# Kernel tuning notes

Hardware: AMD Instinct MI355X
Metric: run time of the kernel (lower is better)

## Reference

```python
import jax, jax.numpy as jnp
import numpy as np

B, S, D = 2, 2048, 2048
H = 16
Q_LORA, KV_LORA = 1536, 512
ROPE_DIM, NOPE_DIM, V_DIM = 64, 64, 128
Q_HEAD_DIM = NOPE_DIM + ROPE_DIM  # 128
ROPE_THETA, ROPE_RATIO = 10000.0, 1.0


def setup_inputs() -> dict:
    key = jax.random.key(0)
    ks = jax.random.split(key, 6)
    std = 0.02
    return {
        "hidden_states": jax.random.normal(ks[0], (B, S, D), jnp.float32),
        "Wqa": jax.random.normal(ks[1], (D, Q_LORA), jnp.float32) * std,
        "Wqb": jax.random.normal(ks[2], (Q_LORA, H * Q_HEAD_DIM), jnp.float32) * std,
        "Wkva": jax.random.normal(ks[3], (D, KV_LORA + ROPE_DIM), jnp.float32) * std,
        "Wkvb": jax.random.normal(ks[4], (KV_LORA, H * (NOPE_DIM + V_DIM)), jnp.float32) * std,
        "Wo": jax.random.normal(ks[5], (H * V_DIM, D), jnp.float32) * std,
    }


def _rope_tables(seq_len):
    half = ROPE_DIM // 2
    inv_freq = ROPE_RATIO / (ROPE_THETA ** (jnp.arange(half, dtype=jnp.float32) * 2.0 / ROPE_DIM))
    freqs = jnp.arange(seq_len, dtype=jnp.float32)[:, None] * inv_freq[None, :]  # [S, half]
    return jnp.cos(freqs), jnp.sin(freqs)


def _apply_rope(x, cos, sin):
    # interleaved even/odd rotation, matches torch stack+flatten
    x_even = x[..., 0::2]
    x_odd = x[..., 1::2]
    r_even = x_even * cos - x_odd * sin
    r_odd = x_odd * cos + x_even * sin
    return jnp.stack([r_even, r_odd], axis=-1).reshape(x.shape)


def reference(hidden_states, Wqa, Wqb, Wkva, Wkvb, Wo):
    b, s, _ = hidden_states.shape
    scale = Q_HEAD_DIM ** -0.5

    # query compression path
    q_latent = hidden_states @ Wqa                             # [B,S,Q_LORA]
    q = (q_latent @ Wqb).reshape(b, s, H, Q_HEAD_DIM)
    q = jnp.transpose(q, (0, 2, 1, 3))                          # [B,H,S,q_head_dim]
    q_nope, q_pe = q[..., :NOPE_DIM], q[..., NOPE_DIM:]

    # kv compression
    kv_comp = hidden_states @ Wkva                              # [B,S,KV_LORA+ROPE]
    c_kv, k_pe = kv_comp[..., :KV_LORA], kv_comp[..., KV_LORA:]

    cos, sin = _rope_tables(s)                                  # [S, ROPE_DIM//2]
    q_pe = _apply_rope(q_pe, cos, sin)                          # [B,H,S,ROPE]
    k_pe = _apply_rope(k_pe, cos, sin)                          # [B,S,ROPE]

    # kv decompression
    kv = (c_kv @ Wkvb).reshape(b, s, H, NOPE_DIM + V_DIM)
    kv = jnp.transpose(kv, (0, 2, 1, 3))                        # [B,H,S,nope+v]
    k_nope, v = kv[..., :NOPE_DIM], kv[..., NOPE_DIM:]

    k_pe_b = jnp.broadcast_to(k_pe[:, None], (b, H, s, ROPE_DIM))
    q_full = jnp.concatenate([q_nope, q_pe], axis=-1)           # [B,H,S,128]
    k_full = jnp.concatenate([k_nope, k_pe_b], axis=-1)         # [B,H,S,128]

    scores = jnp.einsum('bhqd,bhkd->bhqk', q_full, k_full) * scale
    causal = jnp.tril(jnp.ones((s, s), dtype=bool))
    scores = jnp.where(causal[None, None], scores, jnp.finfo(scores.dtype).min)
    probs = jax.nn.softmax(scores, axis=-1)
    attn = jnp.einsum('bhqk,bhkd->bhqd', probs, v)              # [B,H,S,V_DIM]

    out = jnp.transpose(attn, (0, 2, 1, 3)).reshape(b, s, H * V_DIM)
    return out @ Wo                                             # [B,S,D]
```

## Files before the change

kernel.cpp:

```cpp
#include <hip/hip_runtime.h>
#include <hip/hip_bf16.h>
#include <cstdint>
#include <cstddef>

typedef __bf16 bf16_t;
typedef __attribute__((ext_vector_type(4))) __bf16 bf16x4;
typedef __attribute__((ext_vector_type(8))) __bf16 bf16x8;
typedef __attribute__((ext_vector_type(4))) float f32x4;

#define S_ 2048
#define H_ 16
#define NTOK 4096

__device__ __forceinline__ f32x4 mfma16x16(bf16x8 a, bf16x8 b, f32x4 c) {
  return __builtin_amdgcn_mfma_f32_16x16x32_bf16(a, b, c, 0, 0, 0);
}
__device__ __forceinline__ bf16x8 load8(const bf16_t* p) {
  return *reinterpret_cast<const bf16x8*>(p);
}
__device__ __forceinline__ void load_lds16(const void* g, void* l) {
  __builtin_amdgcn_global_load_lds(
      (const __attribute__((address_space(1))) uint32_t*)g,
      (__attribute__((address_space(3))) uint32_t*)l, 16, 0, 0);
}


__global__ void cast_bf16_k(const float* __restrict__ in, bf16_t* __restrict__ out, int n) {
  int idx = blockIdx.x * 256 + threadIdx.x;
  int i4 = idx * 4;
  if (i4 >= n) return;
  float4 v = *reinterpret_cast<const float4*>(in + i4);
  out[i4 + 0] = (bf16_t)v.x;
  out[i4 + 1] = (bf16_t)v.y;
  out[i4 + 2] = (bf16_t)v.z;
  out[i4 + 3] = (bf16_t)v.w;
}

__global__ void rope_tables_k(float* __restrict__ cosT, float* __restrict__ sinT) {
  int idx = blockIdx.x * 256 + threadIdx.x;
  if (idx >= S_ * 32) return;
  int s = idx >> 5, i = idx & 31;
  float inv = powf(10000.0f, -(2.0f * (float)i) / 64.0f);
  float fr = (float)s * inv;
  cosT[idx] = cosf(fr);
  sinT[idx] = sinf(fr);
}

struct TDesc {
  const float* src;
  bf16_t* dst;
  int K, Nsrc, bxc, off, perm;
};
struct TDesc5 {
  TDesc d[5];
};

__global__ void transpose_cast_multi_k(TDesc5 ds) {
  __shared__ float tile[32][33];
  const int bid = blockIdx.x;
  int i = 0;
#pragma unroll
  for (int j = 1; j < 5; ++j)
    if (bid >= ds.d[j].off) i = j;
  const float* __restrict__ in = ds.d[i].src;
  bf16_t* __restrict__ out = ds.d[i].dst;
  const int K = ds.d[i].K, Nsrc = ds.d[i].Nsrc;
  const int local = bid - ds.d[i].off;
  const int n0 = (local % ds.d[i].bxc) * 32;
  const int k0 = (local / ds.d[i].bxc) * 32;
  int srcn0 = n0;
  if (ds.d[i].perm) {
    srcn0 = (n0 < 1024) ? ((n0 >> 6) * 192 + (n0 & 63))
                        : (((n0 - 1024) >> 7) * 192 + 64 + ((n0 - 1024) & 127));
  }
  int tx = threadIdx.x & 31, ty = threadIdx.x >> 5;
#pragma unroll
  for (int r = 0; r < 4; ++r) {
    int k = k0 + ty + r * 8, n = srcn0 + tx;
    tile[ty + r * 8][tx] = (n < Nsrc) ? in[(size_t)k * Nsrc + n] : 0.0f;
  }
  __syncthreads();
#pragma unroll
  for (int r = 0; r < 4; ++r) {
    int n = n0 + ty + r * 8, k = k0 + tx;
    out[(size_t)n * K + k] = (bf16_t)tile[tx][ty + r * 8];
  }
}


__device__ __forceinline__ void gemm_loop(const bf16_t* __restrict__ A, int lda,
                                          const bf16_t* __restrict__ Bt, int K, int m0, int n0,
                                          int tid, bf16_t* Al, bf16_t* Bl, f32x4 (&acc)[4][4]) {
  const int wid = tid >> 6, lane = tid & 63;
  const int wm = (wid >> 1) * 64, wn = (wid & 1) * 64;
  const int srow = wid * 32 + (lane >> 2);
  const int scol = (lane & 3) * 8;
  const bf16_t* ag0 = A + (size_t)(m0 + srow) * lda + scol;
  const bf16_t* ag1 = A + (size_t)(m0 + srow + 16) * lda + scol;
  const bf16_t* bg0 = Bt + (size_t)(n0 + srow) * K + scol;
  const bf16_t* bg1 = Bt + (size_t)(n0 + srow + 16) * K + scol;
  bf16_t* al0 = &Al[wid * 1024];
  bf16_t* al1 = &Al[wid * 1024 + 512];
  bf16_t* bl0 = &Bl[wid * 1024];
  bf16_t* bl1 = &Bl[wid * 1024 + 512];
  const int lr = lane & 15, lk = (lane >> 4) * 8;

  for (int k0 = 0; k0 < K; k0 += 32) {
    load_lds16(ag0 + k0, al0);
    load_lds16(ag1 + k0, al1);
    load_lds16(bg0 + k0, bl0);
    load_lds16(bg1 + k0, bl1);
    __syncthreads();
    bf16x8 af[4], bfr[4];
#pragma unroll
    for (int i = 0; i < 4; ++i) {
      af[i] = load8(&Al[(wm + i * 16 + lr) * 32 + lk]);
      bfr[i] = load8(&Bl[(wn + i * 16 + lr) * 32 + lk]);
    }
#pragma unroll
    for (int i = 0; i < 4; ++i)
#pragma unroll
      for (int j = 0; j < 4; ++j) acc[i][j] = mfma16x16(af[i], bfr[j], acc[i][j]);
    __syncthreads();
  }
}


__global__ __launch_bounds__(256) void gemm_lat_k(const bf16_t* __restrict__ A,
                                                  const bf16_t* __restrict__ Bt,
                                                  bf16_t* __restrict__ C,
                                                  const float* __restrict__ cosT,
                                                  const float* __restrict__ sinT) {
  __shared__ alignas(16) bf16_t Al[128 * 32];
  __shared__ alignas(16) bf16_t Bl[128 * 32];
  const int tid = threadIdx.x;
  const int m0 = blockIdx.y * 128, n0 = blockIdx.x * 128;
  f32x4 acc[4][4] = {};
  gemm_loop(A, 2048, Bt, 2048, m0, n0, tid, Al, Bl, acc);

  const int wid = tid >> 6, lane = tid & 63;
  const int wm = (wid >> 1) * 64, wn = (wid & 1) * 64;
  const int lr = lane & 15, lg = lane >> 4;
  const bool rope = (n0 == 2048) && (wn == 0);
  const int ir_base = lr >> 1;
  const bool odd = lane & 1;
#pragma unroll
  for (int i = 0; i < 4; ++i)
#pragma unroll
    for (int j = 0; j < 4; ++j) {
      float v4[4];
#pragma unroll
      for (int r = 0; r < 4; ++r) v4[r] = acc[i][j][r];
      if (rope) {
        const int ir = j * 8 + ir_base;
#pragma unroll
        for (int r = 0; r < 4; ++r) {
          const int srow_ = (m0 + wm + i * 16 + lg * 4 + r) & (S_ - 1);
          float c = cosT[srow_ * 32 + ir], sn = sinT[srow_ * 32 + ir];
          float partner = __shfl_xor(v4[r], 1);
          v4[r] = odd ? (v4[r] * c + partner * sn) : (v4[r] * c - partner * sn);
        }
      }
#pragma unroll
      for (int r = 0; r < 4; ++r) {
        int row = m0 + wm + i * 16 + lg * 4 + r;
        int col = n0 + wn + j * 16 + lr;
        C[(size_t)row * 2176 + col] = (bf16_t)v4[r];
      }
    }
}


__global__ __launch_bounds__(256) void gemm_qkv_k(const bf16_t* __restrict__ lat,
                                                  const bf16_t* __restrict__ Wqbt,
                                                  const bf16_t* __restrict__ Wkvbt,
                                                  bf16_t* __restrict__ qb,
                                                  bf16_t* __restrict__ knb,
                                                  bf16_t* __restrict__ vT,
                                                  const float* __restrict__ cosT,
                                                  const float* __restrict__ sinT, float qscale) {
  __shared__ alignas(16) bf16_t Al[128 * 32];
  __shared__ alignas(16) bf16_t Bl[128 * 32];
  const int tid = threadIdx.x;
  const int bid = blockIdx.x;
  const int wid = tid >> 6, lane = tid & 63;
  const int wm = (wid >> 1) * 64, wn = (wid & 1) * 64;
  const int lr = lane & 15, lg = lane >> 4;
  f32x4 acc[4][4] = {};

  if (bid < 512) {
    const int m0 = (bid >> 4) * 128, n0 = (bid & 15) * 128;
    gemm_loop(lat, 2176, Wqbt, 1536, m0, n0, tid, Al, Bl, acc);
    const bool rope = (wn == 64);
    const int ir_base = lr >> 1;
    const bool odd = lane & 1;
#pragma unroll
    for (int i = 0; i < 4; ++i)
#pragma unroll
      for (int j = 0; j < 4; ++j) {
        float v4[4];
#pragma unroll
        for (int r = 0; r < 4; ++r) v4[r] = acc[i][j][r] * qscale;
        if (rope) {
          const int ir = j * 8 + ir_base;
#pragma unroll
          for (int r = 0; r < 4; ++r) {
            const int srow_ = (m0 + wm + i * 16 + lg * 4 + r) & (S_ - 1);
            float c = cosT[srow_ * 32 + ir], sn = sinT[srow_ * 32 + ir];
            float partner = __shfl_xor(v4[r], 1);
            v4[r] = odd ? (v4[r] * c + partner * sn) : (v4[r] * c - partner * sn);
          }
        }
#pragma unroll
        for (int r = 0; r < 4; ++r) {
          int row = m0 + wm + i * 16 + lg * 4 + r;
          int col = n0 + wn + j * 16 + lr;
          qb[(size_t)row * 2048 + col] = (bf16_t)v4[r];
        }
      }
  } else {
    const int b2 = bid - 512;
    const int m0 = (b2 / 24) * 128, n0 = (b2 % 24) * 128;
    gemm_loop(lat + 1536, 2176, Wkvbt, 512, m0, n0, tid, Al, Bl, acc);
    if (n0 < 1024) {
#pragma unroll
      for (int i = 0; i < 4; ++i)
#pragma unroll
        for (int j = 0; j < 4; ++j)
#pragma unroll
          for (int r = 0; r < 4; ++r) {
            int row = m0 + wm + i * 16 + lg * 4 + r;
            int col = n0 + wn + j * 16 + lr;
            knb[(size_t)row * 1024 + col] = (bf16_t)acc[i][j][r];
          }
    } else {
#pragma unroll
      for (int i = 0; i < 4; ++i) {
        const int row0 = m0 + wm + i * 16 + lg * 4;
        const int bb = row0 >> 11;
        const int s0 = row0 & (S_ - 1);
#pragma unroll
        for (int j = 0; j < 4; ++j) {
          const int idx = n0 + wn + j * 16 + lr - 1024;
          const int h = idx >> 7, d = idx & 127;
          bf16x4 pk;
#pragma unroll
          for (int r = 0; r < 4; ++r) pk[r] = (bf16_t)acc[i][j][r];
          *reinterpret_cast<bf16x4*>(&vT[((size_t)(bb * 16 + h) * 128 + d) * 2048 + s0]) = pk;
        }
      }
    }
  }
}


__global__ __launch_bounds__(256) void gemm_out_k(const bf16_t* __restrict__ A,
                                                  const bf16_t* __restrict__ Bt,
                                                  float* __restrict__ C) {
  __shared__ alignas(16) bf16_t Al[128 * 32];
  __shared__ alignas(16) bf16_t Bl[128 * 32];
  const int tid = threadIdx.x;
  const int m0 = blockIdx.y * 128, n0 = blockIdx.x * 128;
  f32x4 acc[4][4] = {};
  gemm_loop(A, 2048, Bt, 2048, m0, n0, tid, Al, Bl, acc);
  const int wid = tid >> 6, lane = tid & 63;
  const int wm = (wid >> 1) * 64, wn = (wid & 1) * 64;
  const int lr = lane & 15, lg = lane >> 4;
#pragma unroll
  for (int i = 0; i < 4; ++i)
#pragma unroll
    for (int j = 0; j < 4; ++j)
#pragma unroll
      for (int r = 0; r < 4; ++r) {
        int row = m0 + wm + i * 16 + lg * 4 + r;
        int col = n0 + wn + j * 16 + lr;
        C[(size_t)row * 2048 + col] = acc[i][j][r];
      }
}

__global__ __launch_bounds__(256) void attn_fused(const bf16_t* __restrict__ q,
                                                  const bf16_t* __restrict__ knb,
                                                  const bf16_t* __restrict__ lat,
                                                  const bf16_t* __restrict__ vT,
                                                  bf16_t* __restrict__ out) {
  __shared__ alignas(16) bf16_t Kn[64 * 64];
  __shared__ alignas(16) bf16_t Kp[64 * 64];
  __shared__ alignas(16) bf16_t Vt[128 * 64];
  __shared__ alignas(16) bf16_t Pl[4][16 * 64];
  const int tid = threadIdx.x, wid = tid >> 6, lane = tid & 63;
  const int bid = blockIdx.x;
  const int g = bid >> 8;
  const int x = (bid >> 5) & 7;
  const int bh = bid & 31;
  const int qt = (g & 1) ? (24 - g * 8 + x) : (31 - g * 8 - x);
  const int b = bh >> 4, h = bh & 15;
  const int tokb = b * S_;
  const int lr = lane & 15, lg = lane >> 4;
  const int srow8 = lane >> 3, c8 = lane & 7;
  const int swz8 = c8 ^ srow8;
  bf16_t* Pw = &Pl[wid][0];

  bf16x8 ones;
#pragma unroll
  for (int j = 0; j < 8; ++j) ones[j] = (bf16_t)1.0f;

  bf16x8 qf[4];
  {
    const int qrow = qt * 64 + wid * 16 + lr;
    const bf16_t* qp = q + (size_t)(tokb + qrow) * 2048 + h * 128 + lg * 8;
#pragma unroll
    for (int ds = 0; ds < 4; ++ds) qf[ds] = load8(qp + ds * 32);
  }

  f32x4 o[8] = {};
  f32x4 o8 = {};
  float mrow[4] = {-1e30f, -1e30f, -1e30f, -1e30f};

  for (int t = 0; t <= qt; ++t) {
    const int kb = t * 64;
#pragma unroll
    for (int rr = 0; rr < 2; ++rr) {
      const int r0 = wid * 16 + rr * 8;
      const size_t tk = (size_t)(tokb + kb + r0 + srow8);
      load_lds16(knb + tk * 1024 + h * 64 + (swz8 << 3), &Kn[r0 * 64]);
      load_lds16(lat + tk * 2176 + 2048 + (swz8 << 3), &Kp[r0 * 64]);
    }
#pragma unroll
    for (int rr = 0; rr < 4; ++rr) {
      const int r0 = wid * 32 + rr * 8;
      load_lds16(vT + ((size_t)bh * 128 + r0 + srow8) * 2048 + kb + (swz8 << 3), &Vt[r0 * 64]);
    }
    __syncthreads();

    f32x4 s[4];
    __builtin_amdgcn_s_setprio(1);
#pragma unroll
    for (int kt = 0; kt < 4; ++kt) {
      const int row = kt * 16 + lr;
      const int e = lr & 7;
      bf16x8 kf0 = load8(&Kn[row * 64 + ((lg ^ e) << 3)]);
      bf16x8 kf1 = load8(&Kn[row * 64 + (((lg + 4) ^ e) << 3)]);
      bf16x8 kf2 = load8(&Kp[row * 64 + ((lg ^ e) << 3)]);
      bf16x8 kf3 = load8(&Kp[row * 64 + (((lg + 4) ^ e) << 3)]);
      f32x4 acc = {0.f, 0.f, 0.f, 0.f};
      acc = mfma16x16(qf[0], kf0, acc);
      acc = mfma16x16(qf[1], kf1, acc);
      acc = mfma16x16(qf[2], kf2, acc);
      acc = mfma16x16(qf[3], kf3, acc);
      s[kt] = acc;
    }
    __builtin_amdgcn_s_setprio(0);

    if (t == qt) {
#pragma unroll
      for (int kt = 0; kt < 4; ++kt) {
        const int key = kb + kt * 16 + lr;
#pragma unroll
        for (int r = 0; r < 4; ++r) {
          const int qr = qt * 64 + wid * 16 + lg * 4 + r;
          if (key > qr) s[kt][r] = -1e30f;
        }
      }
    }

    float tm[4];
#pragma unroll
    for (int r = 0; r < 4; ++r) {
      float mx = fmaxf(fmaxf(s[0][r], s[1][r]), fmaxf(s[2][r], s[3][r]));
      mx = fmaxf(mx, __shfl_xor(mx, 1));
      mx = fmaxf(mx, __shfl_xor(mx, 2));
      mx = fmaxf(mx, __shfl_xor(mx, 4));
      mx = fmaxf(mx, __shfl_xor(mx, 8));
      tm[r] = mx;
    }
    float need = fmaxf(fmaxf(tm[0] - mrow[0], tm[1] - mrow[1]),
                       fmaxf(tm[2] - mrow[2], tm[3] - mrow[3]));
    if (!__all(need <= 8.0f)) {
#pragma unroll
      for (int r = 0; r < 4; ++r) {
        float mn = fmaxf(mrow[r], tm[r]);
        float corr = exp2f(mrow[r] - mn);
        mrow[r] = mn;
        o8[r] *= corr;
#pragma unroll
        for (int n = 0; n < 8; ++n) o[n][r] *= corr;
      }
    }
#pragma unroll
    for (int kt = 0; kt < 4; ++kt)
#pragma unroll
      for (int r = 0; r < 4; ++r) s[kt][r] = exp2f(s[kt][r] - mrow[r]);

#pragma unroll
    for (int kt = 0; kt < 4; ++kt)
#pragma unroll
      for (int r = 0; r < 4; ++r) {
        const int qrow = lg * 4 + r;
        const int key = kt * 16 + lr;
        Pw[qrow * 64 + ((((key >> 3) ^ (qrow & 7)) << 3) | (key & 7))] = (bf16_t)s[kt][r];
      }

    __builtin_amdgcn_s_setprio(1);
#pragma unroll
    for (int ks = 0; ks < 2; ++ks) {
      const int e = lr & 7;
      bf16x8 pa = load8(&Pw[lr * 64 + (((ks * 4 + lg) ^ e) << 3)]);
#pragma unroll
      for (int n = 0; n < 8; ++n) {
        bf16x8 vb = load8(&Vt[(n * 16 + lr) * 64 + (((ks * 4 + lg) ^ e) << 3)]);
        o[n] = mfma16x16(pa, vb, o[n]);
      }
      o8 = mfma16x16(pa, ones, o8);
    }
    __builtin_amdgcn_s_setprio(0);
    __syncthreads();
  }

  float linv[4];
#pragma unroll
  for (int r = 0; r < 4; ++r) linv[r] = __builtin_amdgcn_rcpf(o8[r]);
#pragma unroll
  for (int n = 0; n < 8; ++n)
#pragma unroll
    for (int r = 0; r < 4; ++r) {
      const int qr = qt * 64 + wid * 16 + lg * 4 + r;
      out[(size_t)(tokb + qr) * 2048 + h * 128 + n * 16 + lr] = (bf16_t)(o[n][r] * linv[r]);
    }
}


extern "C" void kernel_launch(void* const* d_in, const int* in_sizes, int n_in, void* d_out,
                              int out_size, void* d_ws, size_t ws_size, hipStream_t stream) {
  const float* hs = (const float*)d_in[0];
  const float* Wqa = (const float*)d_in[1];
  const float* Wqb = (const float*)d_in[2];
  const float* Wkva = (const float*)d_in[3];
  const float* Wkvb = (const float*)d_in[4];
  const float* Wo = (const float*)d_in[5];
  float* out = (float*)d_out;

  char* ws = (char*)d_ws;
  size_t off = 0;
  auto alloc = [&](size_t bytes) {
    void* p = ws + off;
    off += (bytes + 255) & ~(size_t)255;
    return p;
  };
  bf16_t* hsb = (bf16_t*)alloc((size_t)NTOK * 2048 * 2);
  bf16_t* W1t = (bf16_t*)alloc((size_t)2176 * 2048 * 2);
  bf16_t* Wqbt = (bf16_t*)alloc((size_t)2048 * 1536 * 2);
  bf16_t* Wkvbt = (bf16_t*)alloc((size_t)3072 * 512 * 2);
  bf16_t* Wot = (bf16_t*)alloc((size_t)2048 * 2048 * 2);
  bf16_t* lat = (bf16_t*)alloc((size_t)NTOK * 2176 * 2);
  bf16_t* qb = (bf16_t*)alloc((size_t)NTOK * 2048 * 2);
  bf16_t* knb = (bf16_t*)alloc((size_t)NTOK * 1024 * 2);
  bf16_t* attn = (bf16_t*)alloc((size_t)NTOK * 2048 * 2);
  bf16_t* vT = (bf16_t*)alloc((size_t)32 * 128 * 2048 * 2);
  float* cosT = (float*)alloc((size_t)S_ * 32 * 4);
  float* sinT = (float*)alloc((size_t)S_ * 32 * 4);

  cast_bf16_k<<<(NTOK * 2048 / 4 + 255) / 256, 256, 0, stream>>>(hs, hsb, NTOK * 2048);
  rope_tables_k<<<(S_ * 32 + 255) / 256, 256, 0, stream>>>(cosT, sinT);
  {
    TDesc5 ds;
    int o0 = 0;
    auto add = [&](int i, const float* src, bf16_t* dst, int K, int Nsrc, int Nout, int perm) {
      int bxc = Nout / 32, cnt = bxc * (K / 32);
      ds.d[i] = TDesc{src, dst, K, Nsrc, bxc, o0, perm};
      o0 += cnt;
    };
    add(0, Wqa, W1t, 2048, 1536, 1536, 0);
    add(1, Wkva, W1t + (size_t)1536 * 2048, 2048, 576, 640, 0);
    add(2, Wqb, Wqbt, 1536, 2048, 2048, 0);
    add(3, Wkvb, Wkvbt, 512, 3072, 3072, 1);
    add(4, Wo, Wot, 2048, 2048, 2048, 0);
    transpose_cast_multi_k<<<o0, 256, 0, stream>>>(ds);
  }

  gemm_lat_k<<<dim3(17, 32), 256, 0, stream>>>(hsb, W1t, lat, cosT, sinT);
  const float scale = 0.08838834764831845f * 1.4426950408889634f;
  gemm_qkv_k<<<dim3(1280), 256, 0, stream>>>(lat, Wqbt, Wkvbt, qb, knb, vT, cosT, sinT, scale);
  attn_fused<<<dim3(1024), 256, 0, stream>>>(qb, knb, lat, vT, attn);
  gemm_out_k<<<dim3(16, 32), 256, 0, stream>>>(attn, Wot, out);
}
```

Before: 306.7 us.

## Use K=64 LDS tiles with XOR swizzle and XCD-aware block remapping in GEMMs

The shared GEMM main loop now stages 64-wide K slices instead of 32, halving the number of barrier pairs per K, and applies an XOR swizzle to the LDS layout to avoid bank conflicts on the fragment reads. The three GEMM kernels also switch to 1D grids with a block-index remap that groups tiles by blockIdx modulo 8, intended to keep neighbouring tiles on the same XCD for better L2 reuse. LDS use per block doubles to 32 KB, which may reduce occupancy.

```diff
diff --git a/kernel.cpp b/kernel.cpp
--- a/kernel.cpp
+++ b/kernel.cpp
@@ -88,39 +88,39 @@
 }
 
 
-__device__ __forceinline__ void gemm_loop(const bf16_t* __restrict__ A, int lda,
-                                          const bf16_t* __restrict__ Bt, int K, int m0, int n0,
-                                          int tid, bf16_t* Al, bf16_t* Bl, f32x4 (&acc)[4][4]) {
+__device__ __forceinline__ void gemm_loop64(const bf16_t* __restrict__ A, int lda,
+                                            const bf16_t* __restrict__ Bt, int K, int m0, int n0,
+                                            int tid, bf16_t* Al, bf16_t* Bl, f32x4 (&acc)[4][4]) {
   const int wid = tid >> 6, lane = tid & 63;
   const int wm = (wid >> 1) * 64, wn = (wid & 1) * 64;
-  const int srow = wid * 32 + (lane >> 2);
-  const int scol = (lane & 3) * 8;
-  const bf16_t* ag0 = A + (size_t)(m0 + srow) * lda + scol;
-  const bf16_t* ag1 = A + (size_t)(m0 + srow + 16) * lda + scol;
-  const bf16_t* bg0 = Bt + (size_t)(n0 + srow) * K + scol;
-  const bf16_t* bg1 = Bt + (size_t)(n0 + srow + 16) * K + scol;
-  bf16_t* al0 = &Al[wid * 1024];
-  bf16_t* al1 = &Al[wid * 1024 + 512];
-  bf16_t* bl0 = &Bl[wid * 1024];
-  bf16_t* bl1 = &Bl[wid * 1024 + 512];
-  const int lr = lane & 15, lk = (lane >> 4) * 8;
-
-  for (int k0 = 0; k0 < K; k0 += 32) {
-    load_lds16(ag0 + k0, al0);
-    load_lds16(ag1 + k0, al1);
-    load_lds16(bg0 + k0, bl0);
-    load_lds16(bg1 + k0, bl1);
+  const int srow8 = lane >> 3, c8 = lane & 7;
+  const int swz8 = c8 ^ srow8;
+  const int lr = lane & 15, lg = lane >> 4;
+  const int e = lr & 7;
+
+  const bf16_t* ag = A + (size_t)(m0 + wid * 32 + srow8) * lda + (swz8 << 3);
+  const bf16_t* bg = Bt + (size_t)(n0 + wid * 32 + srow8) * K + (swz8 << 3);
+
+  for (int k0 = 0; k0 < K; k0 += 64) {
+#pragma unroll
+    for (int rr = 0; rr < 4; ++rr) {
+      load_lds16(ag + (size_t)(rr * 8) * lda + k0, &Al[(wid * 32 + rr * 8) * 64]);
+      load_lds16(bg + (size_t)(rr * 8) * K + k0, &Bl[(wid * 32 + rr * 8) * 64]);
+    }
     __syncthreads();
-    bf16x8 af[4], bfr[4];
-#pragma unroll
-    for (int i = 0; i < 4; ++i) {
-      af[i] = load8(&Al[(wm + i * 16 + lr) * 32 + lk]);
-      bfr[i] = load8(&Bl[(wn + i * 16 + lr) * 32 + lk]);
-    }
-#pragma unroll
-    for (int i = 0; i < 4; ++i)
-#pragma unroll
-      for (int j = 0; j < 4; ++j) acc[i][j] = mfma16x16(af[i], bfr[j], acc[i][j]);
+#pragma unroll
+    for (int kk = 0; kk < 2; ++kk) {
+      bf16x8 af[4], bfr[4];
+#pragma unroll
+      for (int i = 0; i < 4; ++i) {
+        af[i] = load8(&Al[(wm + i * 16 + lr) * 64 + (((kk * 4 + lg) ^ e) << 3)]);
+        bfr[i] = load8(&Bl[(wn + i * 16 + lr) * 64 + (((kk * 4 + lg) ^ e) << 3)]);
+      }
+#pragma unroll
+      for (int i = 0; i < 4; ++i)
+#pragma unroll
+        for (int j = 0; j < 4; ++j) acc[i][j] = mfma16x16(af[i], bfr[j], acc[i][j]);
+    }
     __syncthreads();
   }
 }
@@ -131,12 +131,13 @@
                                                   bf16_t* __restrict__ C,
                                                   const float* __restrict__ cosT,
                                                   const float* __restrict__ sinT) {
-  __shared__ alignas(16) bf16_t Al[128 * 32];
-  __shared__ alignas(16) bf16_t Bl[128 * 32];
+  __shared__ alignas(16) bf16_t Al[128 * 64];
+  __shared__ alignas(16) bf16_t Bl[128 * 64];
   const int tid = threadIdx.x;
-  const int m0 = blockIdx.y * 128, n0 = blockIdx.x * 128;
+  const int sw = (blockIdx.x & 7) * 68 + (blockIdx.x >> 3);
+  const int m0 = (sw / 17) * 128, n0 = (sw % 17) * 128;
   f32x4 acc[4][4] = {};
-  gemm_loop(A, 2048, Bt, 2048, m0, n0, tid, Al, Bl, acc);
+  gemm_loop64(A, 2048, Bt, 2048, m0, n0, tid, Al, Bl, acc);
 
   const int wid = tid >> 6, lane = tid & 63;
   const int wm = (wid >> 1) * 64, wn = (wid & 1) * 64;
@@ -179,18 +180,18 @@
                                                   bf16_t* __restrict__ vT,
                                                   const float* __restrict__ cosT,
                                                   const float* __restrict__ sinT, float qscale) {
-  __shared__ alignas(16) bf16_t Al[128 * 32];
-  __shared__ alignas(16) bf16_t Bl[128 * 32];
+  __shared__ alignas(16) bf16_t Al[128 * 64];
+  __shared__ alignas(16) bf16_t Bl[128 * 64];
   const int tid = threadIdx.x;
-  const int bid = blockIdx.x;
+  const int sw = (blockIdx.x & 7) * 160 + (blockIdx.x >> 3);
   const int wid = tid >> 6, lane = tid & 63;
   const int wm = (wid >> 1) * 64, wn = (wid & 1) * 64;
   const int lr = lane & 15, lg = lane >> 4;
   f32x4 acc[4][4] = {};
 
-  if (bid < 512) {
-    const int m0 = (bid >> 4) * 128, n0 = (bid & 15) * 128;
-    gemm_loop(lat, 2176, Wqbt, 1536, m0, n0, tid, Al, Bl, acc);
+  if (sw < 512) {
+    const int m0 = (sw >> 4) * 128, n0 = (sw & 15) * 128;
+    gemm_loop64(lat, 2176, Wqbt, 1536, m0, n0, tid, Al, Bl, acc);
     const bool rope = (wn == 64);
     const int ir_base = lr >> 1;
     const bool odd = lane & 1;
@@ -219,9 +220,9 @@
         }
       }
   } else {
-    const int b2 = bid - 512;
+    const int b2 = sw - 512;
     const int m0 = (b2 / 24) * 128, n0 = (b2 % 24) * 128;
-    gemm_loop(lat + 1536, 2176, Wkvbt, 512, m0, n0, tid, Al, Bl, acc);
+    gemm_loop64(lat + 1536, 2176, Wkvbt, 512, m0, n0, tid, Al, Bl, acc);
     if (n0 < 1024) {
 #pragma unroll
       for (int i = 0; i < 4; ++i)
@@ -257,12 +258,13 @@
 __global__ __launch_bounds__(256) void gemm_out_k(const bf16_t* __restrict__ A,
                                                   const bf16_t* __restrict__ Bt,
                                                   float* __restrict__ C) {
-  __shared__ alignas(16) bf16_t Al[128 * 32];
-  __shared__ alignas(16) bf16_t Bl[128 * 32];
+  __shared__ alignas(16) bf16_t Al[128 * 64];
+  __shared__ alignas(16) bf16_t Bl[128 * 64];
   const int tid = threadIdx.x;
-  const int m0 = blockIdx.y * 128, n0 = blockIdx.x * 128;
+  const int sw = (blockIdx.x & 7) * 64 + (blockIdx.x >> 3);
+  const int m0 = (sw >> 4) * 128, n0 = (sw & 15) * 128;
   f32x4 acc[4][4] = {};
-  gemm_loop(A, 2048, Bt, 2048, m0, n0, tid, Al, Bl, acc);
+  gemm_loop64(A, 2048, Bt, 2048, m0, n0, tid, Al, Bl, acc);
   const int wid = tid >> 6, lane = tid & 63;
   const int wm = (wid >> 1) * 64, wn = (wid & 1) * 64;
   const int lr = lane & 15, lg = lane >> 4;
@@ -477,9 +479,9 @@
     transpose_cast_multi_k<<<o0, 256, 0, stream>>>(ds);
   }
 
-  gemm_lat_k<<<dim3(17, 32), 256, 0, stream>>>(hsb, W1t, lat, cosT, sinT);
+  gemm_lat_k<<<dim3(544), 256, 0, stream>>>(hsb, W1t, lat, cosT, sinT);
   const float scale = 0.08838834764831845f * 1.4426950408889634f;
   gemm_qkv_k<<<dim3(1280), 256, 0, stream>>>(lat, Wqbt, Wkvbt, qb, knb, vT, cosT, sinT, scale);
   attn_fused<<<dim3(1024), 256, 0, stream>>>(qb, knb, lat, vT, attn);
-  gemm_out_k<<<dim3(16, 32), 256, 0, stream>>>(attn, Wot, out);
-}
+  gemm_out_k<<<dim3(512), 256, 0, stream>>>(attn, Wot, out);
+}
```

Measured after the change: 305.4 us. Within noise of the previous version (-0.4%).
